# Kernel optimization log

Hardware: AMD Instinct MI355X
Metric: run time of the kernel (lower is better)

Reference implementation:

```python
import jax, jax.numpy as jnp
import numpy as np

B, N, D, H, M, O = 8, 1024, 256, 512, 256, 256


def _mlp(x, W1, b1, W2, b2):
    # two-layer MLP: Linear -> ReLU -> Linear (torch Linear: x @ W.T + b)
    return jax.nn.relu(x @ W1.T + b1) @ W2.T + b2


def _lstm(x, W_ih, W_hh, b):
    # x: [B, N, D] -> h: [B, N, H]; single-layer unidirectional LSTM, torch gate order i,f,g,o
    Bt, Nt, _ = x.shape
    x_proj = x @ W_ih.T + b  # [B, N, 4H] precompute input projection

    def step(carry, xt):
        h, c = carry
        gates = xt + h @ W_hh.T
        i, f, g, o = jnp.split(gates, 4, axis=-1)
        i, f, o = jax.nn.sigmoid(i), jax.nn.sigmoid(f), jax.nn.sigmoid(o)
        c = f * c + i * jnp.tanh(g)
        h = o * jnp.tanh(c)
        return (h, c), h

    h0 = jnp.zeros((Bt, W_hh.shape[1]), x.dtype)
    (_, _), hs = jax.lax.scan(step, (h0, h0), jnp.swapaxes(x_proj, 0, 1))
    return jnp.swapaxes(hs, 0, 1)


def setup_inputs() -> dict:
    key = jax.random.key(0)
    ks = jax.random.split(key, 32)
    p = lambda k, s: jax.random.normal(k, s, jnp.float32) * 0.02
    inp = {
        "feats": jax.random.normal(ks[0], (B, N, D), jnp.float32),
        "adj": jax.random.randint(ks[1], (B, N, N), 0, 2, jnp.int32),
        "W_ih": p(ks[2], (4 * H, D)),
        "W_hh": p(ks[3], (4 * H, H)),
        "b_ih": jnp.zeros((4 * H,), jnp.float32),
        "b_hh": jnp.zeros((4 * H,), jnp.float32),
        "gx_W1": p(ks[4], (M, H)), "gx_b1": jnp.zeros((M,), jnp.float32),
        "gx_W2": p(ks[5], (M, M)), "gx_b2": jnp.zeros((M,), jnp.float32),
        "gz_W1": p(ks[6], (M, H)), "gz_b1": jnp.zeros((M,), jnp.float32),
        "gz_W2": p(ks[7], (M, M)), "gz_b2": jnp.zeros((M,), jnp.float32),
        "gv_W1": p(ks[8], (M, H)), "gv_b1": jnp.zeros((M,), jnp.float32),
        "gv_W2": p(ks[9], (M, M)), "gv_b2": jnp.zeros((M,), jnp.float32),
        "gn_W1": p(ks[10], (M, M)), "gn_b1": jnp.zeros((M,), jnp.float32),
        "gn_W2": p(ks[11], (O, M)), "gn_b2": jnp.zeros((O,), jnp.float32),
        "out_W": p(ks[12], (O, H + O)), "out_b": jnp.zeros((O,), jnp.float32),
    }
    return inp


def reference(feats, adj, W_ih, W_hh, b_ih, b_hh,
              gx_W1, gx_b1, gx_W2, gx_b2,
              gz_W1, gz_b1, gz_W2, gz_b2,
              gv_W1, gv_b1, gv_W2, gv_b2,
              gn_W1, gn_b1, gn_W2, gn_b2,
              out_W, out_b):
    h = _lstm(feats, W_ih, W_hh, b_ih + b_hh)  # [B, N, H]

    # Note: in the source, concat_1[:, :lstm_hidden_dim] == s_i and
    # concat_2[:, :lstm_hidden_dim] == s_j, so scores = <g_x(s_i), g_v(s_j)>
    ax = _mlp(h, gx_W1, gx_b1, gx_W2, gx_b2)  # [B, N, M]
    av = _mlp(h, gv_W1, gv_b1, gv_W2, gv_b2)  # [B, N, M]
    scores = jnp.einsum('bim,bjm->bij', ax, av)  # [B, N, N]

    eye = jnp.eye(N, dtype=bool)
    mask = (adj > 0) & ~eye[None]  # valid neighbors
    w = jax.nn.softmax(jnp.where(mask, scores, -1e30), axis=-1)
    w = w * mask  # zero out rows with no neighbors (softmax of all -inf -> uniform)

    sagg = jnp.einsum('bij,bjh->bih', w, h)  # weighted neighbor sum [B, N, H]
    agg = _mlp(_mlp(sagg, gz_W1, gz_b1, gz_W2, gz_b2), gn_W1, gn_b1, gn_W2, gn_b2)
    has_nb = mask.any(axis=-1, keepdims=True)  # [B, N, 1]
    agg = jnp.where(has_nb, agg, 0.0)  # isolated nodes get zero aggregate

    combined = jnp.concatenate([h, agg], axis=-1)  # [B, N, H+O]
    return combined @ out_W.T + out_b
```

## Files before the change

### kernel.cpp

```cpp
#include <hip/hip_runtime.h>

typedef unsigned short u16;
typedef unsigned long long u64;
using short8 = __attribute__((ext_vector_type(8))) short;
using f32x4  = __attribute__((ext_vector_type(4))) float;

#define GF_RELU  1
#define GF_F32   2
#define GF_XPOSE 4

__device__ __forceinline__ float b2f(u16 x) {
    unsigned u = ((unsigned)x) << 16;
    return __builtin_bit_cast(float, u);
}
__device__ __forceinline__ u16 f2b(float f) {
    unsigned u = __builtin_bit_cast(unsigned, f);
    unsigned r = u + 0x7FFFu + ((u >> 16) & 1u);
    return (u16)(r >> 16);
}
__device__ __forceinline__ f32x4 mfma_bf16(uint4 a, uint4 b, f32x4 c) {
    return __builtin_amdgcn_mfma_f32_16x16x32_bf16(
        __builtin_bit_cast(short8, a), __builtin_bit_cast(short8, b), c, 0, 0, 0);
}
__device__ __forceinline__ f32x4 zero4() { f32x4 z = {0.f, 0.f, 0.f, 0.f}; return z; }

__global__ __launch_bounds__(256) void cvt_bf16(const float* __restrict__ src,
                                                u16* __restrict__ dst, int n) {
    for (int i = blockIdx.x * 256 + threadIdx.x; i < n; i += gridDim.x * 256)
        dst[i] = f2b(src[i]);
}

__global__ void pack_params(const float* __restrict__ Whh, const float* __restrict__ Wih,
                            const float* __restrict__ bih, const float* __restrict__ bhh,
                            u16* __restrict__ WhhP, u16* __restrict__ WihP,
                            float* __restrict__ biasP) {
    int p = blockIdx.x;
    int t = threadIdx.x;
    int orig = ((p & 3) << 9) + (p >> 2);
    WhhP[((long)p << 9) + t]       = f2b(Whh[((long)orig << 9) + t]);
    WhhP[((long)p << 9) + 256 + t] = f2b(Whh[((long)orig << 9) + 256 + t]);
    WihP[((long)p << 8) + t]       = f2b(Wih[((long)orig << 8) + t]);
    if (t == 0) biasP[p] = bih[orig] + bhh[orig];
}

__global__ __launch_bounds__(256) void gemm_bt(
    const u16* __restrict__ A, const u16* __restrict__ A2, int ksplit,
    const u16* __restrict__ B, void* __restrict__ Cout,
    int M, int N, int K,
    long sAb, long sBb, long sCb,
    const float* __restrict__ bias, const float* __restrict__ rowmask, int flags) {
    __shared__ __align__(16) u16 As[64][40];
    __shared__ __align__(16) u16 Bs[128][40];
    const int bz = blockIdx.z;
    const u16* Ab = A + (long)bz * sAb;
    const u16* Bb = B + (long)bz * sBb;
    const int m0 = blockIdx.x << 6, n0 = blockIdx.y << 7;
    const int tid = threadIdx.x;
    const int lane = tid & 63, wave = tid >> 6;
    const int srow = tid >> 2, skc = (tid & 3) << 3;
    const int frm = lane & 15, fq = lane >> 4;

    f32x4 acc[8];
#pragma unroll
    for (int i = 0; i < 8; i++) acc[i] = zero4();

    for (int k0 = 0; k0 < K; k0 += 32) {
        int ka = k0 + skc;
        const u16* asrc;
        if (ka < ksplit) asrc = Ab + (long)(m0 + srow) * ksplit + ka;
        else             asrc = A2 + (long)(m0 + srow) * (K - ksplit) + (ka - ksplit);
        uint4 a  = *(const uint4*)asrc;
        uint4 b0 = *(const uint4*)(Bb + (long)(n0 + srow) * K + ka);
        uint4 b1 = *(const uint4*)(Bb + (long)(n0 + 64 + srow) * K + ka);
        __syncthreads();
        *(uint4*)&As[srow][skc] = a;
        *(uint4*)&Bs[srow][skc] = b0;
        *(uint4*)&Bs[64 + srow][skc] = b1;
        __syncthreads();
        uint4 af = *(const uint4*)&As[(wave << 4) + frm][fq << 3];
#pragma unroll
        for (int nt = 0; nt < 8; nt++) {
            uint4 bf = *(const uint4*)&Bs[(nt << 4) + frm][fq << 3];
            acc[nt] = mfma_bf16(af, bf, acc[nt]);
        }
    }
#pragma unroll
    for (int nt = 0; nt < 8; nt++) {
        int col = n0 + (nt << 4) + frm;
        float bv = bias ? bias[col] : 0.f;
#pragma unroll
        for (int r = 0; r < 4; r++) {
            int row = m0 + (wave << 4) + (fq << 2) + r;
            float v = acc[nt][r] + bv;
            if (flags & GF_RELU) v = fmaxf(v, 0.f);
            if (rowmask) v *= rowmask[row];
            long orow = (flags & GF_XPOSE) ? (long)((row & 1023) * 8 + (row >> 10))
                                           : (long)row;
            if (flags & GF_F32)
                ((float*)Cout)[(long)bz * sCb + orow * N + col] = v;
            else
                ((u16*)Cout)[(long)bz * sCb + orow * N + col] = f2b(v);
        }
    }
}

__global__ __launch_bounds__(512, 1) void lstm_rec(
    const u16* __restrict__ WhhP, const u16* __restrict__ xproj,
    u16* __restrict__ h, u64* __restrict__ hx) {
    __shared__ float g_lds[8][260];
    __shared__ unsigned hshare[8][260];
    const int wg = blockIdx.x;
    const int tid = threadIdx.x;
    const int lane = tid & 63, wv = tid >> 6;
    const int frm = lane & 15, fq = lane >> 4;
    const int mbb = frm & 7;
    const int xb = (fq & 1) << 2;
    const int ws = (wg << 3) + wv;

    uint4 bfrag[2][16];
#pragma unroll
    for (int T = 0; T < 2; T++)
#pragma unroll
        for (int kk = 0; kk < 16; kk++)
            bfrag[T][kk] = *(const uint4*)&WhhP[((long)((ws << 5) + (T << 4) + frm) << 9) +
                                                (kk << 5) + (fq << 3)];

    float creg = 0.f;
    int budget = 1 << 21;

#pragma unroll 1
    for (int t = 0; t < 1024; t++) {
        float xp[2][4];
#pragma unroll
        for (int T = 0; T < 2; T++)
#pragma unroll
            for (int r = 0; r < 4; r++)
                xp[T][r] = b2f(xproj[((long)(t * 8 + xb + r) << 11) +
                                     (ws << 5) + (T << 4) + frm]);

        f32x4 acc0 = zero4(), acc1 = zero4();
        if (t > 0) {
            const u64* buf = hx + (((t - 1) & 1) << 11);
            u64 v[4];
            const unsigned want = (unsigned)t;
            while (true) {
#pragma unroll
                for (int j = 0; j < 4; j++)
                    v[j] = __hip_atomic_load(&buf[(wv << 8) + lane + (j << 6)],
                                             __ATOMIC_RELAXED, __HIP_MEMORY_SCOPE_AGENT);
                bool ok = true;
#pragma unroll
                for (int j = 0; j < 4; j++) ok &= ((unsigned)(v[j] >> 32) == want);
                if (__all(ok) || --budget < 0) break;
            }
#pragma unroll
            for (int j = 0; j < 4; j++) {
                int a = (wv << 8) + lane + (j << 6);
                hshare[a >> 8][a & 255] = (unsigned)v[j];
            }
            __syncthreads();
            uint4 afr[16];
#pragma unroll
            for (int kk = 0; kk < 16; kk++)
                afr[kk] = *(const uint4*)&hshare[mbb][(kk << 4) + (fq << 2)];
#pragma unroll
            for (int kk = 0; kk < 16; kk++) {
                acc0 = mfma_bf16(afr[kk], bfrag[0][kk], acc0);
                acc1 = mfma_bf16(afr[kk], bfrag[1][kk], acc1);
            }
        }

        if (fq < 2) {
#pragma unroll
            for (int T = 0; T < 2; T++) {
                f32x4 accT = T ? acc1 : acc0;
#pragma unroll
                for (int r = 0; r < 4; r++)
                    g_lds[(fq << 2) + r][(wv << 5) + (T << 4) + frm] = accT[r] + xp[T][r];
            }
        }
        __syncthreads();

        {
            f32x4 g = *(const f32x4*)&g_lds[wv][lane << 2];
            float iv = 1.f / (1.f + __expf(-g[0]));
            float fv = 1.f / (1.f + __expf(-g[1]));
            float gv = 1.f - 2.f / (__expf(2.f * g[2]) + 1.f);
            float ov = 1.f / (1.f + __expf(-g[3]));
            creg = fv * creg + iv * gv;
            float hv = ov * (1.f - 2.f / (__expf(2.f * creg) + 1.f));
            float hn = __shfl_down(hv, 1);
            if (!(lane & 1)) {
                int b = wv, j = lane >> 1;
                unsigned dw = (unsigned)f2b(hv) | ((unsigned)f2b(hn) << 16);
                ((unsigned*)h)[(((long)(b * 1024 + t)) << 8) + (wg << 5) + j] = dw;
                u64 pv = ((u64)(unsigned)(t + 1) << 32) | (u64)dw;
                __hip_atomic_store(&hx[((t & 1) << 11) + (b << 8) + (wg << 5) + j], pv,
                                   __ATOMIC_RELAXED, __HIP_MEMORY_SCOPE_AGENT);
            }
        }
    }
}

__global__ __launch_bounds__(256) void transpose_h(const u16* __restrict__ h,
                                                   u16* __restrict__ hT) {
    __shared__ __align__(16) u16 tile[64][72];
    const int b = blockIdx.z;
    const int t0 = blockIdx.x << 6, u0 = blockIdx.y << 6;
    const int tid = threadIdx.x;
    const int r = tid >> 3, c8 = (tid & 7) << 3;
#pragma unroll
    for (int j = 0; j < 2; j++) {
        int row = r + (j << 5);
        *(uint4*)&tile[row][c8] =
            *(const uint4*)&h[(((long)b << 10) + t0 + row) * 512 + u0 + c8];
    }
    __syncthreads();
#pragma unroll
    for (int j = 0; j < 2; j++) {
        int urow = r + (j << 5);
        unsigned wds[4];
#pragma unroll
        for (int k = 0; k < 4; k++) {
            unsigned lo = tile[c8 + (k << 1)][urow];
            unsigned hi = tile[c8 + (k << 1) + 1][urow];
            wds[k] = lo | (hi << 16);
        }
        uint4 v; v.x = wds[0]; v.y = wds[1]; v.z = wds[2]; v.w = wds[3];
        *(uint4*)&hT[(((long)b << 9) + u0 + urow) * 1024 + t0 + c8] = v;
    }
}

__global__ __launch_bounds__(256) void softmax_row(
    const float* __restrict__ scores, const int* __restrict__ adj,
    u16* __restrict__ w, float* __restrict__ hasnb) {
    __shared__ float red[4];
    const int row = blockIdx.x;
    const int i = row & 1023;
    const int tid = threadIdx.x;
    const int lane = tid & 63, wave = tid >> 6;
    const float* s = scores + ((long)row << 10);
    const int* arow = adj + ((long)row << 10);

    float sv[4]; bool mk[4];
    float mx = -3.0e38f;
#pragma unroll
    for (int q = 0; q < 4; q++) {
        int j = tid + (q << 8);
        mk[q] = (arow[j] > 0) && (j != i);
        sv[q] = s[j];
        if (mk[q]) mx = fmaxf(mx, sv[q]);
    }
    for (int off = 32; off; off >>= 1) mx = fmaxf(mx, __shfl_xor(mx, off));
    if (lane == 0) red[wave] = mx;
    __syncthreads();
    mx = fmaxf(fmaxf(red[0], red[1]), fmaxf(red[2], red[3]));
    float e[4]; float sum = 0.f;
#pragma unroll
    for (int q = 0; q < 4; q++) {
        e[q] = mk[q] ? __expf(sv[q] - mx) : 0.f;
        sum += e[q];
    }
    __syncthreads();
    for (int off = 32; off; off >>= 1) sum += __shfl_xor(sum, off);
    if (lane == 0) red[wave] = sum;
    __syncthreads();
    sum = red[0] + red[1] + red[2] + red[3];
    float inv = sum > 0.f ? 1.f / sum : 0.f;
#pragma unroll
    for (int q = 0; q < 4; q++) {
        int j = tid + (q << 8);
        w[((long)row << 10) + j] = f2b(e[q] * inv);
    }
    if (tid == 0) hasnb[row] = sum > 0.f ? 1.f : 0.f;
}

extern "C" void kernel_launch(void* const* d_in, const int* in_sizes, int n_in,
                              void* d_out, int out_size, void* d_ws, size_t ws_size,
                              hipStream_t stream) {
    const float* feats = (const float*)d_in[0];
    const int*   adj   = (const int*)d_in[1];
    const float* W_ih  = (const float*)d_in[2];
    const float* W_hh  = (const float*)d_in[3];
    const float* b_ih  = (const float*)d_in[4];
    const float* b_hh  = (const float*)d_in[5];
    const float* gx_W1 = (const float*)d_in[6];  const float* gx_b1 = (const float*)d_in[7];
    const float* gx_W2 = (const float*)d_in[8];  const float* gx_b2 = (const float*)d_in[9];
    const float* gz_W1 = (const float*)d_in[10]; const float* gz_b1 = (const float*)d_in[11];
    const float* gz_W2 = (const float*)d_in[12]; const float* gz_b2 = (const float*)d_in[13];
    const float* gv_W1 = (const float*)d_in[14]; const float* gv_b1 = (const float*)d_in[15];
    const float* gv_W2 = (const float*)d_in[16]; const float* gv_b2 = (const float*)d_in[17];
    const float* gn_W1 = (const float*)d_in[18]; const float* gn_b1 = (const float*)d_in[19];
    const float* gn_W2 = (const float*)d_in[20]; const float* gn_b2 = (const float*)d_in[21];
    const float* out_W = (const float*)d_in[22]; const float* out_b = (const float*)d_in[23];

    char* ws = (char*)d_ws;
    size_t off = 0;
    auto alloc = [&](size_t bytes) {
        void* p = ws + off;
        off += (bytes + 255) & ~(size_t)255;
        return p;
    };
    u16* WhhP      = (u16*)alloc(2048L * 512 * 2);
    u16* WihP      = (u16*)alloc(2048L * 256 * 2);
    float* biasP   = (float*)alloc(2048L * 4);
    u64* hx        = (u64*)alloc(2L * 2048 * 8);
    u16* featsB    = (u16*)alloc(8192L * 256 * 2);
    u16* gxW1b     = (u16*)alloc(256L * 512 * 2);
    u16* gxW2b     = (u16*)alloc(256L * 256 * 2);
    u16* gvW1b     = (u16*)alloc(256L * 512 * 2);
    u16* gvW2b     = (u16*)alloc(256L * 256 * 2);
    u16* gzW1b     = (u16*)alloc(256L * 512 * 2);
    u16* gzW2b     = (u16*)alloc(256L * 256 * 2);
    u16* gnW1b     = (u16*)alloc(256L * 256 * 2);
    u16* gnW2b     = (u16*)alloc(256L * 256 * 2);
    u16* outWb     = (u16*)alloc(256L * 768 * 2);
    u16* xproj     = (u16*)alloc(8L * 1024 * 2048 * 2);
    u16* h         = (u16*)alloc(8L * 1024 * 512 * 2);
    u16* hT        = (u16*)alloc(8L * 1024 * 512 * 2);
    u16* t1        = (u16*)alloc(8192L * 256 * 2);
    u16* tB        = (u16*)alloc(8192L * 256 * 2);
    u16* ax        = (u16*)alloc(8192L * 256 * 2);
    u16* av        = (u16*)alloc(8192L * 256 * 2);
    u16* agg       = (u16*)alloc(8192L * 256 * 2);
    float* hasnb   = (float*)alloc(8192L * 4);
    float* scores  = (float*)alloc(8L * 1024 * 1024 * 4);
    u16* w         = (u16*)alloc(8L * 1024 * 1024 * 2);
    if (off > ws_size) return;

    hipMemsetAsync(hx, 0, 2L * 2048 * 8, stream);
    pack_params<<<2048, 256, 0, stream>>>(W_hh, W_ih, b_ih, b_hh, WhhP, WihP, biasP);

    auto cvt = [&](const float* src, u16* dst, int n) {
        cvt_bf16<<<(n + 1023) / 1024, 256, 0, stream>>>(src, dst, n);
    };
    cvt(feats, featsB, 8192 * 256);
    cvt(gx_W1, gxW1b, 256 * 512);  cvt(gx_W2, gxW2b, 256 * 256);
    cvt(gv_W1, gvW1b, 256 * 512);  cvt(gv_W2, gvW2b, 256 * 256);
    cvt(gz_W1, gzW1b, 256 * 512);  cvt(gz_W2, gzW2b, 256 * 256);
    cvt(gn_W1, gnW1b, 256 * 256);  cvt(gn_W2, gnW2b, 256 * 256);
    cvt(out_W, outWb, 256 * 768);

    gemm_bt<<<dim3(128, 16, 1), 256, 0, stream>>>(
        featsB, nullptr, 256, WihP, xproj, 8192, 2048, 256, 0, 0, 0,
        biasP, nullptr, GF_XPOSE);

    lstm_rec<<<8, 512, 0, stream>>>(WhhP, xproj, h, hx);

    transpose_h<<<dim3(16, 8, 8), 256, 0, stream>>>(h, hT);

    gemm_bt<<<dim3(128, 2, 1), 256, 0, stream>>>(
        h, nullptr, 512, gxW1b, t1, 8192, 256, 512, 0, 0, 0, gx_b1, nullptr, GF_RELU);
    gemm_bt<<<dim3(128, 2, 1), 256, 0, stream>>>(
        t1, nullptr, 256, gxW2b, ax, 8192, 256, 256, 0, 0, 0, gx_b2, nullptr, 0);
    gemm_bt<<<dim3(128, 2, 1), 256, 0, stream>>>(
        h, nullptr, 512, gvW1b, t1, 8192, 256, 512, 0, 0, 0, gv_b1, nullptr, GF_RELU);
    gemm_bt<<<dim3(128, 2, 1), 256, 0, stream>>>(
        t1, nullptr, 256, gvW2b, av, 8192, 256, 256, 0, 0, 0, gv_b2, nullptr, 0);

    gemm_bt<<<dim3(16, 8, 8), 256, 0, stream>>>(
        ax, nullptr, 256, av, scores, 1024, 1024, 256,
        262144, 262144, 1048576, nullptr, nullptr, GF_F32);

    softmax_row<<<8192, 256, 0, stream>>>(scores, adj, w, hasnb);

    u16* sagg = xproj;
    gemm_bt<<<dim3(16, 4, 8), 256, 0, stream>>>(
        w, nullptr, 1024, hT, sagg, 1024, 512, 1024,
        1048576, 524288, 524288, nullptr, nullptr, 0);

    gemm_bt<<<dim3(128, 2, 1), 256, 0, stream>>>(
        sagg, nullptr, 512, gzW1b, t1, 8192, 256, 512, 0, 0, 0, gz_b1, nullptr, GF_RELU);
    gemm_bt<<<dim3(128, 2, 1), 256, 0, stream>>>(
        t1, nullptr, 256, gzW2b, tB, 8192, 256, 256, 0, 0, 0, gz_b2, nullptr, 0);
    gemm_bt<<<dim3(128, 2, 1), 256, 0, stream>>>(
        tB, nullptr, 256, gnW1b, t1, 8192, 256, 256, 0, 0, 0, gn_b1, nullptr, GF_RELU);
    gemm_bt<<<dim3(128, 2, 1), 256, 0, stream>>>(
        t1, nullptr, 256, gnW2b, agg, 8192, 256, 256, 0, 0, 0, gn_b2, hasnb, 0);

    gemm_bt<<<dim3(128, 2, 1), 256, 0, stream>>>(
        h, agg, 512, outWb, (float*)d_out, 8192, 256, 768, 0, 0, 0, out_b, nullptr, GF_F32);
}
```

Measured before the change: 2.463 ms.

## Halve LSTM recurrence workgroups and add register prefetch to GEMM

The LSTM recurrent kernel now runs on 4 workgroups instead of 8, so each wave handles 64 gate columns (four MFMA tiles) and each thread updates two hidden units. This cuts the number of cross-workgroup spin-wait participants per timestep and the global flag traffic, at the cost of doubled per-wave MFMA work and register pressure from 64 B-fragment registers. Separately, the tiled GEMM prefetches the next K-slice from global memory into registers before the MFMA loop, overlapping load latency with compute.

Measured after the change: 5.786 ms. 2.35x slower.

```diff
diff --git a/kernel.cpp b/kernel.cpp
--- a/kernel.cpp
+++ b/kernel.cpp
@@ -60,23 +60,35 @@
     const int srow = tid >> 2, skc = (tid & 3) << 3;
     const int frm = lane & 15, fq = lane >> 4;
 
+    auto loadA = [&](int ka) -> uint4 {
+        const u16* p = (ka < ksplit)
+            ? Ab + (long)(m0 + srow) * ksplit + ka
+            : A2 + (long)(m0 + srow) * (K - ksplit) + (ka - ksplit);
+        return *(const uint4*)p;
+    };
+    const u16* Brow0 = Bb + (long)(n0 + srow) * K;
+    const u16* Brow1 = Bb + (long)(n0 + 64 + srow) * K;
+
     f32x4 acc[8];
 #pragma unroll
     for (int i = 0; i < 8; i++) acc[i] = zero4();
 
+    uint4 a  = loadA(skc);
+    uint4 b0 = *(const uint4*)(Brow0 + skc);
+    uint4 b1 = *(const uint4*)(Brow1 + skc);
+
     for (int k0 = 0; k0 < K; k0 += 32) {
-        int ka = k0 + skc;
-        const u16* asrc;
-        if (ka < ksplit) asrc = Ab + (long)(m0 + srow) * ksplit + ka;
-        else             asrc = A2 + (long)(m0 + srow) * (K - ksplit) + (ka - ksplit);
-        uint4 a  = *(const uint4*)asrc;
-        uint4 b0 = *(const uint4*)(Bb + (long)(n0 + srow) * K + ka);
-        uint4 b1 = *(const uint4*)(Bb + (long)(n0 + 64 + srow) * K + ka);
         __syncthreads();
         *(uint4*)&As[srow][skc] = a;
         *(uint4*)&Bs[srow][skc] = b0;
         *(uint4*)&Bs[64 + srow][skc] = b1;
         __syncthreads();
+        int kn = k0 + 32;
+        if (kn < K) {
+            a  = loadA(kn + skc);
+            b0 = *(const uint4*)(Brow0 + kn + skc);
+            b1 = *(const uint4*)(Brow1 + kn + skc);
+        }
         uint4 af = *(const uint4*)&As[(wave << 4) + frm][fq << 3];
 #pragma unroll
         for (int nt = 0; nt < 8; nt++) {
@@ -107,7 +119,7 @@
 __global__ __launch_bounds__(512, 1) void lstm_rec(
     const u16* __restrict__ WhhP, const u16* __restrict__ xproj,
     u16* __restrict__ h, u64* __restrict__ hx) {
-    __shared__ float g_lds[8][260];
+    __shared__ float g_lds[8][516];
     __shared__ unsigned hshare[8][260];
     const int wg = blockIdx.x;
     const int tid = threadIdx.x;
@@ -115,30 +127,34 @@
     const int frm = lane & 15, fq = lane >> 4;
     const int mbb = frm & 7;
     const int xb = (fq & 1) << 2;
-    const int ws = (wg << 3) + wv;
-
-    uint4 bfrag[2][16];
-#pragma unroll
-    for (int T = 0; T < 2; T++)
+    const int C0 = (wg << 9) + (wv << 6);
+    const int pb = tid >> 6, pj = tid & 63;
+
+    uint4 bfrag[4][16];
+#pragma unroll
+    for (int S = 0; S < 4; S++)
 #pragma unroll
         for (int kk = 0; kk < 16; kk++)
-            bfrag[T][kk] = *(const uint4*)&WhhP[((long)((ws << 5) + (T << 4) + frm) << 9) +
+            bfrag[S][kk] = *(const uint4*)&WhhP[((long)(C0 + (S << 4) + frm) << 9) +
                                                 (kk << 5) + (fq << 3)];
 
-    float creg = 0.f;
+    float creg0 = 0.f, creg1 = 0.f;
     int budget = 1 << 21;
 
 #pragma unroll 1
     for (int t = 0; t < 1024; t++) {
-        float xp[2][4];
-#pragma unroll
-        for (int T = 0; T < 2; T++)
+        float xp[4][4];
+#pragma unroll
+        for (int S = 0; S < 4; S++)
 #pragma unroll
             for (int r = 0; r < 4; r++)
-                xp[T][r] = b2f(xproj[((long)(t * 8 + xb + r) << 11) +
-                                     (ws << 5) + (T << 4) + frm]);
-
-        f32x4 acc0 = zero4(), acc1 = zero4();
+                xp[S][r] = b2f(xproj[((long)(t * 8 + xb + r) << 11) +
+                                     C0 + (S << 4) + frm]);
+
+        f32x4 acc[4];
+#pragma unroll
+        for (int S = 0; S < 4; S++) acc[S] = zero4();
+
         if (t > 0) {
             const u64* buf = hx + (((t - 1) & 1) << 11);
             u64 v[4];
@@ -159,45 +175,45 @@
                 hshare[a >> 8][a & 255] = (unsigned)v[j];
             }
             __syncthreads();
-            uint4 afr[16];
-#pragma unroll
-            for (int kk = 0; kk < 16; kk++)
-                afr[kk] = *(const uint4*)&hshare[mbb][(kk << 4) + (fq << 2)];
 #pragma unroll
             for (int kk = 0; kk < 16; kk++) {
-                acc0 = mfma_bf16(afr[kk], bfrag[0][kk], acc0);
-                acc1 = mfma_bf16(afr[kk], bfrag[1][kk], acc1);
+                uint4 af = *(const uint4*)&hshare[mbb][(kk << 4) + (fq << 2)];
+                acc[0] = mfma_bf16(af, bfrag[0][kk], acc[0]);
+                acc[1] = mfma_bf16(af, bfrag[1][kk], acc[1]);
+                acc[2] = mfma_bf16(af, bfrag[2][kk], acc[2]);
+                acc[3] = mfma_bf16(af, bfrag[3][kk], acc[3]);
             }
         }
 
         if (fq < 2) {
 #pragma unroll
-            for (int T = 0; T < 2; T++) {
-                f32x4 accT = T ? acc1 : acc0;
+            for (int S = 0; S < 4; S++)
 #pragma unroll
                 for (int r = 0; r < 4; r++)
-                    g_lds[(fq << 2) + r][(wv << 5) + (T << 4) + frm] = accT[r] + xp[T][r];
-            }
+                    g_lds[(fq << 2) + r][(wv << 6) + (S << 4) + frm] = acc[S][r] + xp[S][r];
         }
         __syncthreads();
 
         {
-            f32x4 g = *(const f32x4*)&g_lds[wv][lane << 2];
-            float iv = 1.f / (1.f + __expf(-g[0]));
-            float fv = 1.f / (1.f + __expf(-g[1]));
-            float gv = 1.f - 2.f / (__expf(2.f * g[2]) + 1.f);
-            float ov = 1.f / (1.f + __expf(-g[3]));
-            creg = fv * creg + iv * gv;
-            float hv = ov * (1.f - 2.f / (__expf(2.f * creg) + 1.f));
-            float hn = __shfl_down(hv, 1);
-            if (!(lane & 1)) {
-                int b = wv, j = lane >> 1;
-                unsigned dw = (unsigned)f2b(hv) | ((unsigned)f2b(hn) << 16);
-                ((unsigned*)h)[(((long)(b * 1024 + t)) << 8) + (wg << 5) + j] = dw;
-                u64 pv = ((u64)(unsigned)(t + 1) << 32) | (u64)dw;
-                __hip_atomic_store(&hx[((t & 1) << 11) + (b << 8) + (wg << 5) + j], pv,
-                                   __ATOMIC_RELAXED, __HIP_MEMORY_SCOPE_AGENT);
-            }
+            f32x4 ga = *(const f32x4*)&g_lds[pb][pj << 3];
+            f32x4 gb = *(const f32x4*)&g_lds[pb][(pj << 3) + 4];
+            float i0 = 1.f / (1.f + __expf(-ga[0]));
+            float f0 = 1.f / (1.f + __expf(-ga[1]));
+            float c0 = 1.f - 2.f / (__expf(2.f * ga[2]) + 1.f);
+            float o0 = 1.f / (1.f + __expf(-ga[3]));
+            creg0 = f0 * creg0 + i0 * c0;
+            float h0 = o0 * (1.f - 2.f / (__expf(2.f * creg0) + 1.f));
+            float i1 = 1.f / (1.f + __expf(-gb[0]));
+            float f1 = 1.f / (1.f + __expf(-gb[1]));
+            float c1 = 1.f - 2.f / (__expf(2.f * gb[2]) + 1.f);
+            float o1 = 1.f / (1.f + __expf(-gb[3]));
+            creg1 = f1 * creg1 + i1 * c1;
+            float h1 = o1 * (1.f - 2.f / (__expf(2.f * creg1) + 1.f));
+            unsigned dw = (unsigned)f2b(h0) | ((unsigned)f2b(h1) << 16);
+            ((unsigned*)h)[(((long)(pb * 1024 + t)) << 8) + (wg << 6) + pj] = dw;
+            u64 pv = ((u64)(unsigned)(t + 1) << 32) | (u64)dw;
+            __hip_atomic_store(&hx[((t & 1) << 11) + (pb << 8) + (wg << 6) + pj], pv,
+                               __ATOMIC_RELAXED, __HIP_MEMORY_SCOPE_AGENT);
         }
     }
 }
@@ -345,7 +361,7 @@
         featsB, nullptr, 256, WihP, xproj, 8192, 2048, 256, 0, 0, 0,
         biasP, nullptr, GF_XPOSE);
 
-    lstm_rec<<<8, 512, 0, stream>>>(WhhP, xproj, h, hx);
+    lstm_rec<<<4, 512, 0, stream>>>(WhhP, xproj, h, hx);
 
     transpose_h<<<dim3(16, 8, 8), 256, 0, stream>>>(h, hT);
 
```
